# Optimization experiments

Hardware: AMD Instinct MI355X
Metric: run time of the kernel (lower is better)

## Reference

```python
import jax, jax.numpy as jnp
import numpy as np

NA, NB, NG = 100000, 400000, 5000
IN, OUT, H = 128, 128, 2
SLOPE = 0.2
BN_EPS = 1e-5


def setup_inputs() -> dict:
    key = jax.random.key(0)
    ks = jax.random.split(key, 12)
    return {
        "atom_feats": jax.random.normal(ks[0], (NA, IN), jnp.float32),
        "bond_feats": jax.random.normal(ks[1], (NB, IN), jnp.float32),
        "global_feats": jax.random.normal(ks[2], (NG, IN), jnp.float32),
        "W_atom": jax.random.normal(ks[3], (IN, OUT * H), jnp.float32) * 0.05,
        "W_bond": jax.random.normal(ks[4], (IN, OUT * H), jnp.float32) * 0.05,
        "W_global": jax.random.normal(ks[5], (IN, OUT * H), jnp.float32) * 0.05,
        "attn_l": jax.random.normal(ks[6], (1, H, OUT), jnp.float32) * 0.1,
        "attn_r": jax.random.normal(ks[7], (1, H, OUT), jnp.float32) * 0.1,
        "bn_gamma": jnp.ones((OUT,), jnp.float32),
        "bn_beta": jnp.zeros((OUT,), jnp.float32),
        "src": jax.random.randint(ks[8], (NB,), 0, NA, jnp.int32),
        "dst": jax.random.randint(ks[9], (NB,), 0, NA, jnp.int32),
        "gid": jax.random.randint(ks[10], (NA,), 0, NG, jnp.int32),
    }


def _lrelu(x):
    return jnp.where(x >= 0, x, SLOPE * x)


def reference(atom_feats, bond_feats, global_feats, W_atom, W_bond, W_global,
              attn_l, attn_r, bn_gamma, bn_beta, src, dst, gid):
    Na = atom_feats.shape[0]
    # bias-free single-layer MLPs, reshape to [N, heads, out]
    h = (atom_feats @ W_atom).reshape(-1, H, OUT)      # [Na,H,D]
    e = (bond_feats @ W_bond).reshape(-1, H, OUT)      # [Nb,H,D]
    u = (global_feats @ W_global).reshape(-1, H, OUT)  # [Ng,H,D]

    er = (h * attn_r).sum(-1, keepdims=True)    # [Na,H,1]
    el_h = (h * attn_l).sum(-1, keepdims=True)  # [Na,H,1]
    el_e = (e * attn_l).sum(-1, keepdims=True)  # [Nb,H,1]
    el_u = (u * attn_l).sum(-1, keepdims=True)  # [Ng,H,1]

    # raw attention logits
    eh = _lrelu(el_h[src] + er[dst])   # bond: u_add_v  [Nb,H,1]
    ee = _lrelu(el_e + er[dst])        # bond: e_add_v  [Nb,H,1]
    eu = _lrelu(el_u[gid] + er)        # g2a: u_add_v (one edge per atom) [Na,H,1]

    # max-stabilized softmax over all incoming edges (bond eh, bond ee, g2a eu)
    emax_b = jax.ops.segment_max(jnp.maximum(eh, ee), dst, num_segments=Na)
    emax = jnp.maximum(emax_b, eu)     # [Na,H,1]; eu finite -> no -inf

    eh = jnp.exp(eh - emax[dst])
    ee = jnp.exp(ee - emax[dst])
    eu = jnp.exp(eu - emax)

    esum = jax.ops.segment_sum(eh + ee, dst, num_segments=Na) + eu  # [Na,H,1]

    alpha_h = eh / esum[dst]
    alpha_e = ee / esum[dst]
    alpha_u = eu / esum

    # weighted aggregation
    out = jax.ops.segment_sum(h[src] * alpha_h + e * alpha_e, dst, num_segments=Na)
    out = out + u[gid] * alpha_u       # [Na,H,D]

    hm = out.mean(axis=1)              # mean over heads -> [Na,D]

    # BatchNorm1d (training-mode batch statistics)
    mean = hm.mean(axis=0)
    var = hm.var(axis=0)
    hn = (hm - mean) / jnp.sqrt(var + BN_EPS) * bn_gamma + bn_beta
    return jax.nn.relu(hn)
```

## Files before the change

### kernel.cpp

```cpp
#include <hip/hip_runtime.h>
#include <hip/hip_bf16.h>
#include <cstdint>

typedef __attribute__((ext_vector_type(8))) short bf16x8;
typedef __attribute__((ext_vector_type(4))) float f32x4;

__device__ __forceinline__ float bf2f(unsigned short u) {
    return __uint_as_float(((unsigned)u) << 16);
}
__device__ __forceinline__ unsigned short f2bf(float x) {
    unsigned u = __float_as_uint(x);
    u += 0x7fffu + ((u >> 16) & 1u);
    return (unsigned short)(u >> 16);
}
__device__ __forceinline__ float lrelu(float x) { return x >= 0.f ? x : 0.2f * x; }

__global__ void packW(const float* __restrict__ W, unsigned short* __restrict__ Wp) {
    int idx = blockIdx.x * 256 + threadIdx.x;
    int k = idx >> 8, n = idx & 255;
    int kk = k >> 5, r = k & 31, quad = r >> 3, j = r & 7;
    Wp[(((kk << 8) + n) * 4 + quad) * 8 + j] = f2bf(W[idx]);
}

__global__ __launch_bounds__(256) void gemm_mfma(
    const float* __restrict__ A, const unsigned short* __restrict__ Wp,
    unsigned short* __restrict__ C, int M,
    const float* __restrict__ attn_l, const float* __restrict__ attn_r,
    float* __restrict__ el, float* __restrict__ er)
{
    __shared__ unsigned short lds[16896];
    const int t = threadIdx.x;
    const int row0 = blockIdx.x * 64;

#pragma unroll
    for (int i = 0; i < 8; i++) {
        int flat = i * 4096 + t * 16;
        int row = flat >> 9;
        int colf = (flat & 511) >> 2;
        float4 v = make_float4(0.f, 0.f, 0.f, 0.f);
        if (row0 + row < M) v = *(const float4*)(A + (size_t)(row0 + row) * 128 + colf);
        unsigned u0 = (unsigned)f2bf(v.x) | ((unsigned)f2bf(v.y) << 16);
        unsigned u1 = (unsigned)f2bf(v.z) | ((unsigned)f2bf(v.w) << 16);
        *(uint2*)(&lds[row * 136 + colf]) = make_uint2(u0, u1);
    }
    __syncthreads();

    const int w = t >> 6, lane = t & 63;
    const int quad = lane >> 4, l16 = lane & 15;
    const int col0w = w * 64;

    f32x4 acc[4][4];
#pragma unroll
    for (int rt = 0; rt < 4; rt++)
#pragma unroll
        for (int ct = 0; ct < 4; ct++) acc[rt][ct] = (f32x4)(0.f);

#pragma unroll
    for (int kk = 0; kk < 4; kk++) {
        bf16x8 af[4], bf[4];
#pragma unroll
        for (int rt = 0; rt < 4; rt++)
            af[rt] = *(const bf16x8*)(&lds[(rt * 16 + l16) * 136 + kk * 32 + quad * 8]);
#pragma unroll
        for (int ct = 0; ct < 4; ct++) {
            int n = col0w + ct * 16 + l16;
            bf[ct] = *(const bf16x8*)(Wp + ((((kk << 8) + n) * 4 + quad) << 3));
        }
#pragma unroll
        for (int rt = 0; rt < 4; rt++)
#pragma unroll
            for (int ct = 0; ct < 4; ct++)
                acc[rt][ct] = __builtin_amdgcn_mfma_f32_16x16x32_bf16(af[rt], bf[ct], acc[rt][ct], 0, 0, 0);
    }
    __syncthreads();

#pragma unroll
    for (int rt = 0; rt < 4; rt++)
#pragma unroll
        for (int ct = 0; ct < 4; ct++) {
#pragma unroll
            for (int r = 0; r < 4; r++) {
                int row = rt * 16 + quad * 4 + r;
                int col = col0w + ct * 16 + l16;
                lds[row * 264 + col] = f2bf(acc[rt][ct][r]);
            }
        }
    __syncthreads();

#pragma unroll
    for (int i = 0; i < 8; i++) {
        int flat = i * 4096 + t * 16;
        int row = flat >> 9;
        int cb = flat & 511;
        uint4 v = *(const uint4*)((const char*)lds + row * 528 + cb);
        int grow = row0 + row;
        bool valid = grow < M;
        if (valid) *(uint4*)((char*)C + (size_t)grow * 512 + cb) = v;

        int ch = cb >> 1;
        float x0 = bf2f((unsigned short)(v.x & 0xffff)), x1 = bf2f((unsigned short)(v.x >> 16));
        float x2 = bf2f((unsigned short)(v.y & 0xffff)), x3 = bf2f((unsigned short)(v.y >> 16));
        float x4 = bf2f((unsigned short)(v.z & 0xffff)), x5 = bf2f((unsigned short)(v.z >> 16));
        float x6 = bf2f((unsigned short)(v.w & 0xffff)), x7 = bf2f((unsigned short)(v.w >> 16));
        float4 al0 = *(const float4*)(attn_l + ch);
        float4 al1 = *(const float4*)(attn_l + ch + 4);
        float dl = x0 * al0.x + x1 * al0.y + x2 * al0.z + x3 * al0.w
                 + x4 * al1.x + x5 * al1.y + x6 * al1.z + x7 * al1.w;
        float dr = 0.f;
        if (er) {
            float4 ar0 = *(const float4*)(attn_r + ch);
            float4 ar1 = *(const float4*)(attn_r + ch + 4);
            dr = x0 * ar0.x + x1 * ar0.y + x2 * ar0.z + x3 * ar0.w
               + x4 * ar1.x + x5 * ar1.y + x6 * ar1.z + x7 * ar1.w;
        }
#pragma unroll
        for (int off = 8; off >= 1; off >>= 1) {
            dl += __shfl_xor(dl, off);
            dr += __shfl_xor(dr, off);
        }
        if ((t & 15) == 0 && valid) {
            int head = (ch >> 7) & 1;
            el[(size_t)grow * 2 + head] = dl;
            if (er) er[(size_t)grow * 2 + head] = dr;
        }
    }
}

__global__ void hist_kernel(const int* __restrict__ dst, int* __restrict__ deg, int Nb) {
    int t = blockIdx.x * blockDim.x + threadIdx.x;
    if (t < Nb) atomicAdd(&deg[dst[t]], 1);
}

__global__ __launch_bounds__(1024) void scan1024(
    const int* __restrict__ deg, int* __restrict__ rowptr, int* __restrict__ wo, int n)
{
    __shared__ int wsum[16];
    int t = threadIdx.x, lane = t & 63, w = t >> 6;
    int carry = 0;
    for (int base = 0; base < n; base += 1024) {
        int i = base + t;
        int v = (i < n) ? deg[i] : 0;
        int x = v;
#pragma unroll
        for (int off = 1; off < 64; off <<= 1) {
            int y = __shfl_up(x, off);
            if (lane >= off) x += y;
        }
        if (lane == 63) wsum[w] = x;
        __syncthreads();
        if (w == 0) {
            int s = (lane < 16) ? wsum[lane] : 0;
#pragma unroll
            for (int off = 1; off < 16; off <<= 1) {
                int y = __shfl_up(s, off);
                if (lane >= off) s += y;
            }
            if (lane < 16) wsum[lane] = s;
        }
        __syncthreads();
        int wofs = (w > 0) ? wsum[w - 1] : 0;
        int incl = carry + wofs + x;
        if (i < n) { rowptr[i + 1] = incl; wo[i] = incl - v; }
        int total = wsum[15];
        __syncthreads();
        carry += total;
    }
    if (t == 0) rowptr[0] = 0;
}

__global__ void fill_kernel(const int* __restrict__ src, const int* __restrict__ dst,
                            const float* __restrict__ er, const float* __restrict__ elh,
                            const float* __restrict__ ele,
                            int* __restrict__ wo, int* __restrict__ sidx,
                            int* __restrict__ eidx, float4* __restrict__ logits, int Nb) {
    int t = blockIdx.x * blockDim.x + threadIdx.x;
    if (t >= Nb) return;
    int d = dst[t], s = src[t];
    int p = atomicAdd(&wo[d], 1);
    float e0 = er[(size_t)d * 2], e1 = er[(size_t)d * 2 + 1];
    float h0 = elh[(size_t)s * 2], h1 = elh[(size_t)s * 2 + 1];
    float l0 = ele[(size_t)t * 2], l1 = ele[(size_t)t * 2 + 1];
    sidx[p] = s;
    eidx[p] = t;
    logits[p] = make_float4(lrelu(h0 + e0), lrelu(h1 + e1), lrelu(l0 + e0), lrelu(l1 + e1));
}

__global__ __launch_bounds__(256) void aggregate(
    const unsigned short* __restrict__ h, const unsigned short* __restrict__ e,
    const unsigned short* __restrict__ u,
    const float* __restrict__ er, const float* __restrict__ elu,
    const int* __restrict__ rowptr, const int* __restrict__ sidx,
    const int* __restrict__ eidx, const float4* __restrict__ logits,
    const int* __restrict__ gid,
    float* __restrict__ hm, int Na)
{
    int wid = (int)((blockIdx.x * (unsigned)blockDim.x + threadIdx.x) >> 6);
    int lane = threadIdx.x & 63;
    if (wid >= Na) return;
    const int a = wid;
    const float er0 = er[(size_t)a * 2], er1 = er[(size_t)a * 2 + 1];
    const int g = gid[a];
    const float eul0 = lrelu(elu[(size_t)g * 2] + er0);
    const float eul1 = lrelu(elu[(size_t)g * 2 + 1] + er1);
    const int rb = rowptr[a], re = rowptr[a + 1];

    float m0 = eul0, m1 = eul1;
    for (int base = rb; base < re; base += 64) {
        int i = base + lane;
        float lm0 = -1e30f, lm1 = -1e30f;
        if (i < re) {
            float4 lg = logits[i];
            lm0 = fmaxf(lg.x, lg.z);
            lm1 = fmaxf(lg.y, lg.w);
        }
#pragma unroll
        for (int off = 32; off >= 1; off >>= 1) {
            lm0 = fmaxf(lm0, __shfl_xor(lm0, off));
            lm1 = fmaxf(lm1, __shfl_xor(lm1, off));
        }
        m0 = fmaxf(m0, lm0);
        m1 = fmaxf(m1, lm1);
    }

    float es0 = __expf(eul0 - m0), es1 = __expf(eul1 - m1);
    const int head = lane >> 5;
    const int d4 = lane << 2;
    float acc0, acc1, acc2, acc3;
    {
        float eu_sel = head ? es1 : es0;
        ushort4 uv = *(const ushort4*)(u + (size_t)g * 256 + d4);
        acc0 = eu_sel * bf2f(uv.x); acc1 = eu_sel * bf2f(uv.y);
        acc2 = eu_sel * bf2f(uv.z); acc3 = eu_sel * bf2f(uv.w);
    }

    for (int base = rb; base < re; base += 64) {
        int n = min(64, re - base);
        float xh0 = 0.f, xh1 = 0.f, xe0 = 0.f, xe1 = 0.f;
        int sv = 0, bv = 0;
        if (lane < n) {
            float4 lg = logits[base + lane];
            xh0 = __expf(lg.x - m0); xh1 = __expf(lg.y - m1);
            xe0 = __expf(lg.z - m0); xe1 = __expf(lg.w - m1);
            sv = sidx[base + lane];
            bv = eidx[base + lane];
        }
        float s0 = xh0 + xe0, s1 = xh1 + xe1;
#pragma unroll
        for (int off = 32; off >= 1; off >>= 1) {
            s0 += __shfl_xor(s0, off);
            s1 += __shfl_xor(s1, off);
        }
        es0 += s0; es1 += s1;

        for (int j = 0; j < n; j++) {
            int s_j = __shfl(sv, j), b_j = __shfl(bv, j);
            float wh0 = __shfl(xh0, j), wh1 = __shfl(xh1, j);
            float we0 = __shfl(xe0, j), we1 = __shfl(xe1, j);
            float wh = head ? wh1 : wh0;
            float we = head ? we1 : we0;
            ushort4 hv = *(const ushort4*)(h + (size_t)s_j * 256 + d4);
            ushort4 ev = *(const ushort4*)(e + (size_t)b_j * 256 + d4);
            acc0 += wh * bf2f(hv.x) + we * bf2f(ev.x);
            acc1 += wh * bf2f(hv.y) + we * bf2f(ev.y);
            acc2 += wh * bf2f(hv.z) + we * bf2f(ev.z);
            acc3 += wh * bf2f(hv.w) + we * bf2f(ev.w);
        }
    }

    float inv = 1.f / (head ? es1 : es0);
    acc0 *= inv; acc1 *= inv; acc2 *= inv; acc3 *= inv;
    float p0 = __shfl(acc0, (lane + 32) & 63);
    float p1 = __shfl(acc1, (lane + 32) & 63);
    float p2 = __shfl(acc2, (lane + 32) & 63);
    float p3 = __shfl(acc3, (lane + 32) & 63);
    if (lane < 32) {
        float4 o = make_float4(0.5f * (acc0 + p0), 0.5f * (acc1 + p1),
                               0.5f * (acc2 + p2), 0.5f * (acc3 + p3));
        *(float4*)(hm + (size_t)a * 128 + d4) = o;
    }
}

__global__ void bnstats(const float* __restrict__ hm, float* __restrict__ sums, int Na) {
    int t = threadIdx.x;
    int c = t & 127, half = t >> 7;
    float s = 0.f, ss = 0.f;
    for (int r = blockIdx.x * 2 + half; r < Na; r += gridDim.x * 2) {
        float v = hm[(size_t)r * 128 + c];
        s += v; ss += v * v;
    }
    atomicAdd(&sums[c], s);
    atomicAdd(&sums[128 + c], ss);
}

__global__ void bnapply(const float* __restrict__ hm, const float* __restrict__ sums,
                        const float* __restrict__ gamma, const float* __restrict__ beta,
                        float* __restrict__ out, int Na) {
    int t = threadIdx.x;
    int c = t & 127, half = t >> 7;
    float invn = 1.f / (float)Na;
    float mean = sums[c] * invn;
    float var = sums[128 + c] * invn - mean * mean;
    float scale = gamma[c] * rsqrtf(var + 1e-5f);
    float shift = beta[c] - mean * scale;
    for (int r = blockIdx.x * 2 + half; r < Na; r += gridDim.x * 2) {
        float v = hm[(size_t)r * 128 + c] * scale + shift;
        out[(size_t)r * 128 + c] = fmaxf(v, 0.f);
    }
}

extern "C" void kernel_launch(void* const* d_in, const int* in_sizes, int n_in,
                              void* d_out, int out_size, void* d_ws, size_t ws_size,
                              hipStream_t stream)
{
    const float* atom   = (const float*)d_in[0];
    const float* bondf  = (const float*)d_in[1];
    const float* globf  = (const float*)d_in[2];
    const float* Wa     = (const float*)d_in[3];
    const float* Wb     = (const float*)d_in[4];
    const float* Wg     = (const float*)d_in[5];
    const float* attn_l = (const float*)d_in[6];
    const float* attn_r = (const float*)d_in[7];
    const float* gamma  = (const float*)d_in[8];
    const float* beta   = (const float*)d_in[9];
    const int* src      = (const int*)d_in[10];
    const int* dst      = (const int*)d_in[11];
    const int* gid      = (const int*)d_in[12];
    const int Na = in_sizes[0] / 128;
    const int Nb = in_sizes[1] / 128;
    const int Ng = in_sizes[2] / 128;

    char* w = (char*)d_ws;
    size_t off = 0;
    auto alloc = [&](size_t bytes) -> void* {
        void* p = w + off;
        off = (off + bytes + 255) & ~(size_t)255;
        return p;
    };
    unsigned short* h   = (unsigned short*)alloc((size_t)Na * 256 * 2);
    unsigned short* e   = (unsigned short*)alloc((size_t)Nb * 256 * 2);
    unsigned short* u   = (unsigned short*)alloc((size_t)Ng * 256 * 2);
    unsigned short* Wpa = (unsigned short*)alloc(32768 * 2);
    unsigned short* Wpb = (unsigned short*)alloc(32768 * 2);
    unsigned short* Wpg = (unsigned short*)alloc(32768 * 2);
    float* er   = (float*)alloc((size_t)Na * 2 * 4);
    float* elh  = (float*)alloc((size_t)Na * 2 * 4);
    float* ele  = (float*)alloc((size_t)Nb * 2 * 4);
    float* elu  = (float*)alloc((size_t)Ng * 2 * 4);
    int* deg    = (int*)alloc((size_t)Na * 4);
    int* rowptr = (int*)alloc((size_t)(Na + 1) * 4);
    int* wo     = (int*)alloc((size_t)Na * 4);
    int* sidx   = (int*)alloc((size_t)Nb * 4);
    int* eidx   = (int*)alloc((size_t)Nb * 4);
    float4* logits = (float4*)alloc((size_t)Nb * 16);
    float* hm   = (float*)alloc((size_t)Na * 128 * 4);
    float* sums = (float*)alloc(256 * 4);

    hipMemsetAsync(deg, 0, (size_t)Na * 4, stream);
    hipMemsetAsync(sums, 0, 256 * 4, stream);

    packW<<<128, 256, 0, stream>>>(Wa, Wpa);
    packW<<<128, 256, 0, stream>>>(Wb, Wpb);
    packW<<<128, 256, 0, stream>>>(Wg, Wpg);

    gemm_mfma<<<(Na + 63) / 64, 256, 0, stream>>>(atom, Wpa, h, Na, attn_l, attn_r, elh, er);
    gemm_mfma<<<(Nb + 63) / 64, 256, 0, stream>>>(bondf, Wpb, e, Nb, attn_l, nullptr, ele, nullptr);
    gemm_mfma<<<(Ng + 63) / 64, 256, 0, stream>>>(globf, Wpg, u, Ng, attn_l, nullptr, elu, nullptr);

    hist_kernel<<<(Nb + 255) / 256, 256, 0, stream>>>(dst, deg, Nb);
    scan1024<<<1, 1024, 0, stream>>>(deg, rowptr, wo, Na);
    fill_kernel<<<(Nb + 255) / 256, 256, 0, stream>>>(src, dst, er, elh, ele,
                                                      wo, sidx, eidx, logits, Nb);

    aggregate<<<(Na + 3) / 4, 256, 0, stream>>>(h, e, u, er, elu,
                                                rowptr, sidx, eidx, logits, gid, hm, Na);
    bnstats<<<256, 256, 0, stream>>>(hm, sums, Na);
    bnapply<<<512, 256, 0, stream>>>(hm, sums, gamma, beta, (float*)d_out, Na);
}
```

Measured before the change: 817.7 us.

## Fuse three GEMMs, fold attention dots into MFMA, parallelize degree scan

Merges the three pack kernels and three GEMM launches into single launches, with blocks dispatched by index to atom, bond or global tiles. The attention-logit dot products move from a post-GEMM shuffle reduction into one extra MFMA per k-step, using precomputed W·attn vectors (W folded with attn_l/attn_r), so the logits now come from fp32-accumulated bf16 inputs rather than from rounded bf16 outputs. The single-block serial scan over 100k degrees becomes a three-stage multi-block scan. It also adds full-tile/tail template specialization. This trades slight numeric differences and extra launches for less epilogue work and better parallelism.

```diff
diff --git a/kernel.cpp b/kernel.cpp
--- a/kernel.cpp
+++ b/kernel.cpp
@@ -15,22 +15,66 @@
 }
 __device__ __forceinline__ float lrelu(float x) { return x >= 0.f ? x : 0.2f * x; }
 
-__global__ void packW(const float* __restrict__ W, unsigned short* __restrict__ Wp) {
-    int idx = blockIdx.x * 256 + threadIdx.x;
+__global__ void packW3(const float* __restrict__ Wa, const float* __restrict__ Wb,
+                       const float* __restrict__ Wg,
+                       unsigned short* __restrict__ Pa, unsigned short* __restrict__ Pb,
+                       unsigned short* __restrict__ Pg) {
+    int gidx = blockIdx.x * 256 + threadIdx.x;
+    int which = gidx >> 15, idx = gidx & 32767;
+    const float* W = (which == 0) ? Wa : (which == 1) ? Wb : Wg;
+    unsigned short* Wp = (which == 0) ? Pa : (which == 1) ? Pb : Pg;
     int k = idx >> 8, n = idx & 255;
     int kk = k >> 5, r = k & 31, quad = r >> 3, j = r & 7;
     Wp[(((kk << 8) + n) * 4 + quad) * 8 + j] = f2bf(W[idx]);
 }
 
-__global__ __launch_bounds__(256) void gemm_mfma(
+__global__ void makeVpack(const float* __restrict__ Wa, const float* __restrict__ Wb,
+                          const float* __restrict__ Wg,
+                          const float* __restrict__ al, const float* __restrict__ ar,
+                          unsigned short* __restrict__ Va, unsigned short* __restrict__ Vb,
+                          unsigned short* __restrict__ Vg) {
+    const float* W = (blockIdx.x == 0) ? Wa : (blockIdx.x == 1) ? Wb : Wg;
+    unsigned short* Vp = (blockIdx.x == 0) ? Va : (blockIdx.x == 1) ? Vb : Vg;
+    __shared__ float sv[128][4];
+    int t = threadIdx.x;
+    int k = t >> 1, hh = t & 1;
+    const float* wp = W + k * 256 + hh * 128;
+    const float* alp = al + hh * 128;
+    const float* arp = ar + hh * 128;
+    float sl = 0.f, sr = 0.f;
+#pragma unroll
+    for (int d = 0; d < 128; d += 4) {
+        float4 wv = *(const float4*)(wp + d);
+        float4 av = *(const float4*)(alp + d);
+        float4 rv = *(const float4*)(arp + d);
+        sl += wv.x * av.x + wv.y * av.y + wv.z * av.z + wv.w * av.w;
+        sr += wv.x * rv.x + wv.y * rv.y + wv.z * rv.z + wv.w * rv.w;
+    }
+    sv[k][hh] = sl;
+    sv[k][2 + hh] = sr;
+    __syncthreads();
+#pragma unroll
+    for (int ii = 0; ii < 16; ii++) {
+        int idx = t * 16 + ii;
+        int j = idx & 7, q = (idx >> 3) & 3, fc = (idx >> 5) & 15, kk = idx >> 9;
+        int kg = kk * 32 + q * 8 + j;
+        float val = (fc < 4) ? sv[kg][fc] : 0.f;
+        Vp[idx] = f2bf(val);
+    }
+}
+
+template<bool TAIL>
+__device__ __forceinline__ void gemm_body(
     const float* __restrict__ A, const unsigned short* __restrict__ Wp,
+    const unsigned short* __restrict__ Vp,
     unsigned short* __restrict__ C, int M,
-    const float* __restrict__ attn_l, const float* __restrict__ attn_r,
-    float* __restrict__ el, float* __restrict__ er)
+    float* __restrict__ el, float* __restrict__ er,
+    unsigned short* lds, int row0)
 {
-    __shared__ unsigned short lds[16896];
     const int t = threadIdx.x;
-    const int row0 = blockIdx.x * 64;
+    const int w = t >> 6, lane = t & 63;
+    const int quad = lane >> 4, l16 = lane & 15;
+    const int col0w = w * 64;
 
 #pragma unroll
     for (int i = 0; i < 8; i++) {
@@ -38,18 +82,15 @@
         int row = flat >> 9;
         int colf = (flat & 511) >> 2;
         float4 v = make_float4(0.f, 0.f, 0.f, 0.f);
-        if (row0 + row < M) v = *(const float4*)(A + (size_t)(row0 + row) * 128 + colf);
+        if (!TAIL || row0 + row < M) v = *(const float4*)(A + (size_t)(row0 + row) * 128 + colf);
         unsigned u0 = (unsigned)f2bf(v.x) | ((unsigned)f2bf(v.y) << 16);
         unsigned u1 = (unsigned)f2bf(v.z) | ((unsigned)f2bf(v.w) << 16);
         *(uint2*)(&lds[row * 136 + colf]) = make_uint2(u0, u1);
     }
     __syncthreads();
 
-    const int w = t >> 6, lane = t & 63;
-    const int quad = lane >> 4, l16 = lane & 15;
-    const int col0w = w * 64;
-
     f32x4 acc[4][4];
+    f32x4 accf = (f32x4)(0.f);
 #pragma unroll
     for (int rt = 0; rt < 4; rt++)
 #pragma unroll
@@ -57,34 +98,46 @@
 
 #pragma unroll
     for (int kk = 0; kk < 4; kk++) {
-        bf16x8 af[4], bf[4];
+        bf16x8 af[4], bfr[4], afw, vfr;
 #pragma unroll
         for (int rt = 0; rt < 4; rt++)
             af[rt] = *(const bf16x8*)(&lds[(rt * 16 + l16) * 136 + kk * 32 + quad * 8]);
+        afw = *(const bf16x8*)(&lds[(w * 16 + l16) * 136 + kk * 32 + quad * 8]);
 #pragma unroll
         for (int ct = 0; ct < 4; ct++) {
             int n = col0w + ct * 16 + l16;
-            bf[ct] = *(const bf16x8*)(Wp + ((((kk << 8) + n) * 4 + quad) << 3));
-        }
+            bfr[ct] = *(const bf16x8*)(Wp + ((((kk << 8) + n) * 4 + quad) << 3));
+        }
+        vfr = *(const bf16x8*)(Vp + ((((kk << 4) + l16) * 4 + quad) << 3));
 #pragma unroll
         for (int rt = 0; rt < 4; rt++)
 #pragma unroll
             for (int ct = 0; ct < 4; ct++)
-                acc[rt][ct] = __builtin_amdgcn_mfma_f32_16x16x32_bf16(af[rt], bf[ct], acc[rt][ct], 0, 0, 0);
+                acc[rt][ct] = __builtin_amdgcn_mfma_f32_16x16x32_bf16(af[rt], bfr[ct], acc[rt][ct], 0, 0, 0);
+        accf = __builtin_amdgcn_mfma_f32_16x16x32_bf16(afw, vfr, accf, 0, 0, 0);
+    }
+
+    {
+        int frow = row0 + w * 16 + quad * 4;
+        if (l16 < 2) {
+#pragma unroll
+            for (int r = 0; r < 4; r++)
+                if (!TAIL || frow + r < M) el[(size_t)(frow + r) * 2 + l16] = accf[r];
+        } else if (l16 < 4 && er) {
+#pragma unroll
+            for (int r = 0; r < 4; r++)
+                if (!TAIL || frow + r < M) er[(size_t)(frow + r) * 2 + (l16 - 2)] = accf[r];
+        }
     }
     __syncthreads();
 
 #pragma unroll
     for (int rt = 0; rt < 4; rt++)
 #pragma unroll
-        for (int ct = 0; ct < 4; ct++) {
-#pragma unroll
-            for (int r = 0; r < 4; r++) {
-                int row = rt * 16 + quad * 4 + r;
-                int col = col0w + ct * 16 + l16;
-                lds[row * 264 + col] = f2bf(acc[rt][ct][r]);
-            }
-        }
+        for (int ct = 0; ct < 4; ct++)
+#pragma unroll
+            for (int r = 0; r < 4; r++)
+                lds[(rt * 16 + quad * 4 + r) * 264 + col0w + ct * 16 + l16] = f2bf(acc[rt][ct][r]);
     __syncthreads();
 
 #pragma unroll
@@ -92,38 +145,34 @@
         int flat = i * 4096 + t * 16;
         int row = flat >> 9;
         int cb = flat & 511;
-        uint4 v = *(const uint4*)((const char*)lds + row * 528 + cb);
         int grow = row0 + row;
-        bool valid = grow < M;
-        if (valid) *(uint4*)((char*)C + (size_t)grow * 512 + cb) = v;
-
-        int ch = cb >> 1;
-        float x0 = bf2f((unsigned short)(v.x & 0xffff)), x1 = bf2f((unsigned short)(v.x >> 16));
-        float x2 = bf2f((unsigned short)(v.y & 0xffff)), x3 = bf2f((unsigned short)(v.y >> 16));
-        float x4 = bf2f((unsigned short)(v.z & 0xffff)), x5 = bf2f((unsigned short)(v.z >> 16));
-        float x6 = bf2f((unsigned short)(v.w & 0xffff)), x7 = bf2f((unsigned short)(v.w >> 16));
-        float4 al0 = *(const float4*)(attn_l + ch);
-        float4 al1 = *(const float4*)(attn_l + ch + 4);
-        float dl = x0 * al0.x + x1 * al0.y + x2 * al0.z + x3 * al0.w
-                 + x4 * al1.x + x5 * al1.y + x6 * al1.z + x7 * al1.w;
-        float dr = 0.f;
-        if (er) {
-            float4 ar0 = *(const float4*)(attn_r + ch);
-            float4 ar1 = *(const float4*)(attn_r + ch + 4);
-            dr = x0 * ar0.x + x1 * ar0.y + x2 * ar0.z + x3 * ar0.w
-               + x4 * ar1.x + x5 * ar1.y + x6 * ar1.z + x7 * ar1.w;
-        }
-#pragma unroll
-        for (int off = 8; off >= 1; off >>= 1) {
-            dl += __shfl_xor(dl, off);
-            dr += __shfl_xor(dr, off);
-        }
-        if ((t & 15) == 0 && valid) {
-            int head = (ch >> 7) & 1;
-            el[(size_t)grow * 2 + head] = dl;
-            if (er) er[(size_t)grow * 2 + head] = dr;
-        }
-    }
+        if (!TAIL || grow < M)
+            *(uint4*)((char*)C + (size_t)grow * 512 + cb) =
+                *(const uint4*)((const char*)lds + row * 528 + cb);
+    }
+}
+
+__global__ __launch_bounds__(256, 4) void gemm_fused(
+    const float* __restrict__ A0, const float* __restrict__ A1, const float* __restrict__ A2,
+    const unsigned short* __restrict__ W0, const unsigned short* __restrict__ W1,
+    const unsigned short* __restrict__ W2,
+    const unsigned short* __restrict__ V0, const unsigned short* __restrict__ V1,
+    const unsigned short* __restrict__ V2,
+    unsigned short* __restrict__ C0, unsigned short* __restrict__ C1,
+    unsigned short* __restrict__ C2,
+    float* __restrict__ el0, float* __restrict__ el1, float* __restrict__ el2,
+    float* __restrict__ er0,
+    int M0, int M1, int M2, int nb0, int nb01)
+{
+    __shared__ unsigned short lds[16896];
+    int b = blockIdx.x;
+    const float* A; const unsigned short* Wp; const unsigned short* Vp;
+    unsigned short* C; float* el; float* er; int M; int row0;
+    if (b < nb0)       { A = A0; Wp = W0; Vp = V0; C = C0; el = el0; er = er0;     M = M0; row0 = b * 64; }
+    else if (b < nb01) { A = A1; Wp = W1; Vp = V1; C = C1; el = el1; er = nullptr; M = M1; row0 = (b - nb0) * 64; }
+    else               { A = A2; Wp = W2; Vp = V2; C = C2; el = el2; er = nullptr; M = M2; row0 = (b - nb01) * 64; }
+    if (row0 + 64 <= M) gemm_body<false>(A, Wp, Vp, C, M, el, er, lds, row0);
+    else                gemm_body<true >(A, Wp, Vp, C, M, el, er, lds, row0);
 }
 
 __global__ void hist_kernel(const int* __restrict__ dst, int* __restrict__ deg, int Nb) {
@@ -131,41 +180,84 @@
     if (t < Nb) atomicAdd(&deg[dst[t]], 1);
 }
 
-__global__ __launch_bounds__(1024) void scan1024(
-    const int* __restrict__ deg, int* __restrict__ rowptr, int* __restrict__ wo, int n)
+__global__ __launch_bounds__(1024) void scan_blocks(
+    const int* __restrict__ deg, int* __restrict__ rowptr, int* __restrict__ wo,
+    int* __restrict__ partials, int n)
 {
     __shared__ int wsum[16];
     int t = threadIdx.x, lane = t & 63, w = t >> 6;
-    int carry = 0;
-    for (int base = 0; base < n; base += 1024) {
-        int i = base + t;
-        int v = (i < n) ? deg[i] : 0;
-        int x = v;
-#pragma unroll
-        for (int off = 1; off < 64; off <<= 1) {
-            int y = __shfl_up(x, off);
-            if (lane >= off) x += y;
-        }
-        if (lane == 63) wsum[w] = x;
-        __syncthreads();
-        if (w == 0) {
-            int s = (lane < 16) ? wsum[lane] : 0;
-#pragma unroll
-            for (int off = 1; off < 16; off <<= 1) {
-                int y = __shfl_up(s, off);
-                if (lane >= off) s += y;
-            }
-            if (lane < 16) wsum[lane] = s;
-        }
-        __syncthreads();
-        int wofs = (w > 0) ? wsum[w - 1] : 0;
-        int incl = carry + wofs + x;
-        if (i < n) { rowptr[i + 1] = incl; wo[i] = incl - v; }
-        int total = wsum[15];
-        __syncthreads();
-        carry += total;
-    }
-    if (t == 0) rowptr[0] = 0;
+    int i0 = blockIdx.x * 4096 + t * 4;
+    int4 v = make_int4(0, 0, 0, 0);
+    if (i0 + 3 < n) v = *(const int4*)(deg + i0);
+    else {
+        if (i0 < n)     v.x = deg[i0];
+        if (i0 + 1 < n) v.y = deg[i0 + 1];
+        if (i0 + 2 < n) v.z = deg[i0 + 2];
+        if (i0 + 3 < n) v.w = deg[i0 + 3];
+    }
+    int tsum = v.x + v.y + v.z + v.w;
+    int x = tsum;
+#pragma unroll
+    for (int off = 1; off < 64; off <<= 1) {
+        int y = __shfl_up(x, off);
+        if (lane >= off) x += y;
+    }
+    if (lane == 63) wsum[w] = x;
+    __syncthreads();
+    if (w == 0) {
+        int s = (lane < 16) ? wsum[lane] : 0;
+#pragma unroll
+        for (int off = 1; off < 16; off <<= 1) {
+            int y = __shfl_up(s, off);
+            if (lane >= off) s += y;
+        }
+        if (lane < 16) wsum[lane] = s;
+    }
+    __syncthreads();
+    int wofs = (w > 0) ? wsum[w - 1] : 0;
+    int e0 = wofs + (x - tsum);
+    int e1 = e0 + v.x, e2 = e1 + v.y, e3 = e2 + v.z;
+    if (i0 < n)     { wo[i0]     = e0; rowptr[i0 + 1] = e1; }
+    if (i0 + 1 < n) { wo[i0 + 1] = e1; rowptr[i0 + 2] = e2; }
+    if (i0 + 2 < n) { wo[i0 + 2] = e2; rowptr[i0 + 3] = e3; }
+    if (i0 + 3 < n) { wo[i0 + 3] = e3; rowptr[i0 + 4] = e3 + v.w; }
+    if (t == 0) partials[blockIdx.x] = wsum[15];
+}
+
+__global__ __launch_bounds__(1024) void scan_partials_k(int* __restrict__ partials, int nb) {
+    __shared__ int wsum[16];
+    int t = threadIdx.x, lane = t & 63, w = t >> 6;
+    int v = (t < nb) ? partials[t] : 0;
+    int x = v;
+#pragma unroll
+    for (int off = 1; off < 64; off <<= 1) {
+        int y = __shfl_up(x, off);
+        if (lane >= off) x += y;
+    }
+    if (lane == 63) wsum[w] = x;
+    __syncthreads();
+    if (w == 0) {
+        int s = (lane < 16) ? wsum[lane] : 0;
+#pragma unroll
+        for (int off = 1; off < 16; off <<= 1) {
+            int y = __shfl_up(s, off);
+            if (lane >= off) s += y;
+        }
+        if (lane < 16) wsum[lane] = s;
+    }
+    __syncthreads();
+    int wofs = (w > 0) ? wsum[w - 1] : 0;
+    if (t < nb) partials[t] = wofs + (x - v);
+}
+
+__global__ void scan_add_k(int* __restrict__ rowptr, int* __restrict__ wo,
+                           const int* __restrict__ partials, int n) {
+    int i = blockIdx.x * 256 + threadIdx.x;
+    if (i >= n) return;
+    int ofs = partials[i >> 12];
+    rowptr[i + 1] += ofs;
+    wo[i] += ofs;
+    if (i == 0) rowptr[0] = 0;
 }
 
 __global__ void fill_kernel(const int* __restrict__ src, const int* __restrict__ dst,
@@ -342,6 +434,9 @@
     unsigned short* Wpa = (unsigned short*)alloc(32768 * 2);
     unsigned short* Wpb = (unsigned short*)alloc(32768 * 2);
     unsigned short* Wpg = (unsigned short*)alloc(32768 * 2);
+    unsigned short* Vpa = (unsigned short*)alloc(4096 * 2);
+    unsigned short* Vpb = (unsigned short*)alloc(4096 * 2);
+    unsigned short* Vpg = (unsigned short*)alloc(4096 * 2);
     float* er   = (float*)alloc((size_t)Na * 2 * 4);
     float* elh  = (float*)alloc((size_t)Na * 2 * 4);
     float* ele  = (float*)alloc((size_t)Nb * 2 * 4);
@@ -349,6 +444,7 @@
     int* deg    = (int*)alloc((size_t)Na * 4);
     int* rowptr = (int*)alloc((size_t)(Na + 1) * 4);
     int* wo     = (int*)alloc((size_t)Na * 4);
+    int* partials = (int*)alloc(1024 * 4);
     int* sidx   = (int*)alloc((size_t)Nb * 4);
     int* eidx   = (int*)alloc((size_t)Nb * 4);
     float4* logits = (float4*)alloc((size_t)Nb * 16);
@@ -358,16 +454,19 @@
     hipMemsetAsync(deg, 0, (size_t)Na * 4, stream);
     hipMemsetAsync(sums, 0, 256 * 4, stream);
 
-    packW<<<128, 256, 0, stream>>>(Wa, Wpa);
-    packW<<<128, 256, 0, stream>>>(Wb, Wpb);
-    packW<<<128, 256, 0, stream>>>(Wg, Wpg);
-
-    gemm_mfma<<<(Na + 63) / 64, 256, 0, stream>>>(atom, Wpa, h, Na, attn_l, attn_r, elh, er);
-    gemm_mfma<<<(Nb + 63) / 64, 256, 0, stream>>>(bondf, Wpb, e, Nb, attn_l, nullptr, ele, nullptr);
-    gemm_mfma<<<(Ng + 63) / 64, 256, 0, stream>>>(globf, Wpg, u, Ng, attn_l, nullptr, elu, nullptr);
+    packW3<<<384, 256, 0, stream>>>(Wa, Wb, Wg, Wpa, Wpb, Wpg);
+    makeVpack<<<3, 256, 0, stream>>>(Wa, Wb, Wg, attn_l, attn_r, Vpa, Vpb, Vpg);
+
+    const int ba = (Na + 63) / 64, bb = (Nb + 63) / 64, bg = (Ng + 63) / 64;
+    gemm_fused<<<ba + bb + bg, 256, 0, stream>>>(
+        atom, bondf, globf, Wpa, Wpb, Wpg, Vpa, Vpb, Vpg,
+        h, e, u, elh, ele, elu, er, Na, Nb, Ng, ba, ba + bb);
 
     hist_kernel<<<(Nb + 255) / 256, 256, 0, stream>>>(dst, deg, Nb);
-    scan1024<<<1, 1024, 0, stream>>>(deg, rowptr, wo, Na);
+    const int nchunks = (Na + 4095) / 4096;
+    scan_blocks<<<nchunks, 1024, 0, stream>>>(deg, rowptr, wo, partials, Na);
+    scan_partials_k<<<1, 1024, 0, stream>>>(partials, nchunks);
+    scan_add_k<<<(Na + 255) / 256, 256, 0, stream>>>(rowptr, wo, partials, Na);
     fill_kernel<<<(Nb + 255) / 256, 256, 0, stream>>>(src, dst, er, elh, ele,
                                                       wo, sidx, eidx, logits, Nb);
 
```

New measurement: 720.9 us. 11.8% less time.
